# Optimization experiments

Hardware: AMD Instinct MI355X
Metric: run time of the kernel (lower is better)

## Reference

```python
import jax, jax.numpy as jnp
import numpy as np

B, T, D_IN, H, A, DEPTH = 64, 256, 256, 512, 128, 4


def hsig(v):
    # Keras hard_sigmoid
    return jnp.clip(0.2 * v + 0.5, 0.0, 1.0)


def setup_inputs() -> dict:
    key = jax.random.key(0)
    ks = jax.random.split(key, 8)
    s = 0.02
    return {
        "x": jax.random.normal(ks[0], (B, T, D_IN), jnp.float32),
        "mask": jnp.ones((B, T), jnp.float32),
        "bucket_size": T,
        "W_emb": jax.random.normal(ks[1], (D_IN, H), jnp.float32) * s,
        "b_emb": jnp.zeros((H,), jnp.float32),
        "W": jax.random.normal(ks[2], (H, 3 * H), jnp.float32) * s,
        "U": jax.random.normal(ks[3], (H, 3 * H), jnp.float32) * s,
        "b": jnp.zeros((3 * H,), jnp.float32),
        "W_action_1": jax.random.normal(ks[4], (H, A), jnp.float32) * s,
        "U_action_1": jax.random.normal(ks[5], (H, A), jnp.float32) * s,
        "b_action_1": jnp.zeros((A,), jnp.float32),
        "W_action_2": jax.random.normal(ks[6], (A, 2), jnp.float32) * s,
        "b_action_2": jnp.zeros((2,), jnp.float32),
    }


def _forward(x, mask, bucket_size, W_emb, b_emb, W, U, b,
             W_action_1, U_action_1, b_action_1, W_action_2, b_action_2):
    Bn, Tn = x.shape[0], int(bucket_size)
    Hn = W_emb.shape[1]
    f32 = x.dtype

    dm = mask.T[:Tn]                                   # [T,B]
    eos = dm * (1.0 - jnp.concatenate([dm[1:], jnp.zeros((1, Bn), f32)], 0))
    seos = jnp.concatenate([jnp.zeros((1, Bn), f32), eos[:-1]], 0)
    xe = (jnp.einsum('btd,dh->tbh', x, W_emb) + b_emb)[:Tn]  # [T,B,H]
    llm3 = jnp.concatenate([jnp.zeros((DEPTH - 1, Bn), f32), jnp.ones((1, Bn), f32)], 0)

    Wz, Wr, Wh = W[:, :Hn], W[:, Hn:2 * Hn], W[:, 2 * Hn:]
    Uz, Ur, Uh = U[:, :Hn], U[:, Hn:2 * Hn], U[:, 2 * Hn:]
    bz, br, bh = b[:Hn], b[Hn:2 * Hn], b[2 * Hn:]

    def vert_step(carry, llm):
        x_d, ap_d, dm_d = carry                        # [T,B,H],[T,B],[T,B]
        sdm = jnp.concatenate([jnp.ones((1, Bn), f32), dm_d[:-1]], 0)

        def horiz(c, s):
            h_tm1, a_tm1, dmc_tm1 = c
            xt, ap, dmp_tm1, dmp, e_tm1 = s
            pol_h = jax.nn.relu(xt @ W_action_1 + h_tm1 @ U_action_1 + b_action_1)
            pol = jnp.exp(pol_h @ W_action_2 + b_action_2)          # [B,2]
            act = (pol[:, 0] >= pol[:, 1]).astype(f32)
            act = jnp.where(ap > 0, 1.0, act)
            act = jnp.where(llm > 0, 1.0, act)
            act = jnp.where(e_tm1 > 0, 0.0, act)
            act_calc = dmp_tm1 * (1 - llm) * (1 - e_tm1) * (1 - ap)
            z = hsig(xt @ Wz + h_tm1 @ Uz + bz)
            r = hsig(xt @ Wr + h_tm1 @ Ur + br)
            h_cand = z * h_tm1 + (1 - z) * jnp.tanh(xt @ Wh + (r * h_tm1) @ Uh + bh)
            both = (1 - ap) * dmp * act * dmc_tm1
            h_only = dmc_tm1 * act * (ap + (1 - ap) * (1 - dmp))
            x_only = dmp * (1 - ap) * (1 - act + act * (1 - dmc_tm1))
            dm_new = both + x_only + h_only
            h = jnp.where(both[:, None] > 0, h_cand, 0.0)
            h = jnp.where(h_only[:, None] > 0, h_tm1, h)
            h = jnp.where(x_only[:, None] > 0, xt, h)
            act = jnp.where(dmp_tm1 > 0, act, a_tm1)
            dm_new = dmp * dm_new
            h = jnp.where(dmp[:, None] > 0, h, h_tm1)
            return (h, act, dm_new), (h, act, dm_new, act_calc, pol)

        init = (jnp.zeros((Bn, Hn), f32), jnp.zeros((Bn,), f32), jnp.zeros((Bn,), f32))
        _, (h, act, ndm, ac, pol) = jax.lax.scan(horiz, init, (x_d, ap_d, sdm, dm_d, seos))
        sa = jnp.concatenate([act[1:], jnp.zeros((1, Bn), f32)], 0)
        pih = jnp.concatenate([jnp.zeros((1, Bn, Hn), f32), h[1:]], 0)
        return (h, sa, ndm), (h, sa, ac, x_d, pih, pol)

    init = (xe, jnp.zeros((Tn, Bn), f32), dm)
    _, (hS, saS, acS, pixS, pihS, polS) = jax.lax.scan(vert_step, init, llm3)
    output = hS[-1, -1]                                # [B,H]
    action = jnp.transpose(saS, (2, 0, 1))             # [B,depth,T]
    action_calc = jnp.transpose(acS, (2, 0, 1))
    pix = jnp.transpose(pixS, (2, 0, 1, 3))            # [B,depth,T,H]
    pih = jnp.transpose(pihS, (2, 0, 1, 3))
    pol = jnp.transpose(polS, (2, 0, 1, 3))            # [B,depth,T,2]
    return (output, action, action_calc, pix, pih, pol)


def reference(x, mask, bucket_size, W_emb, b_emb, W, U, b,
              W_action_1, U_action_1, b_action_1, W_action_2, b_action_2):
    return _forward(x, mask, bucket_size, W_emb, b_emb, W, U, b,
                    W_action_1, U_action_1, b_action_1, W_action_2, b_action_2)
```

## Files before the change

kernel.cpp:

```cpp
#include <hip/hip_runtime.h>


#define Bn   64
#define Tn   256
#define DIN  256
#define Hn   512
#define An   128
#define DEP  4
#define N3   1536
#define NC   1664
#define NU   1152
#define THREADS 320

__device__ __forceinline__ float hsigf(float v) {
    return fminf(fmaxf(0.2f * v + 0.5f, 0.f), 1.f);
}
__device__ __forceinline__ float aloadf(const float* p) {
    return __hip_atomic_load(p, __ATOMIC_RELAXED, __HIP_MEMORY_SCOPE_AGENT);
}
__device__ __forceinline__ void astoref(float* p, float v) {
    __hip_atomic_store(p, v, __ATOMIC_RELAXED, __HIP_MEMORY_SCOPE_AGENT);
}

__global__ __launch_bounds__(256) void pack_w_k(const float* __restrict__ W,
                                                const float* __restrict__ Wa1,
                                                float* __restrict__ Wc) {
    int idx = blockIdx.x * 256 + threadIdx.x;
    if (idx >= Hn * NC) return;
    int k = idx / NC, c = idx % NC;
    Wc[idx] = (c < N3) ? W[(size_t)k * N3 + c] : Wa1[(size_t)k * An + (c - N3)];
}

__global__ __launch_bounds__(256) void pack_u_k(const float* __restrict__ U,
                                                const float* __restrict__ Ua1,
                                                float* __restrict__ Uc) {
    int idx = blockIdx.x * 256 + threadIdx.x;
    if (idx >= Hn * NU) return;
    int k = idx / NU, c = idx % NU;
    Uc[idx] = (c < 1024) ? U[(size_t)k * N3 + c] : Ua1[(size_t)k * An + (c - 1024)];
}

__global__ __launch_bounds__(256) void init_misc_k(const float* __restrict__ bb,
                                                   const float* __restrict__ ba1,
                                                   float* __restrict__ bc,
                                                   const float* __restrict__ mask,
                                                   float* __restrict__ seos,
                                                   float* __restrict__ dmh0,
                                                   float* __restrict__ o_pih,
                                                   unsigned int* __restrict__ flags) {
    int idx = blockIdx.x * 256 + threadIdx.x;
    if (idx < NC) bc[idx] = (idx < N3) ? bb[idx] : ba1[idx - N3];
    if (idx < 128) flags[idx] = 0u;
    if (idx < Tn * Bn) {
        int t = idx / Bn, b = idx % Bn;
        float m0 = mask[(size_t)b * Tn + t];
        dmh0[idx] = m0;
        float s = 0.f;
        if (t > 0) s = mask[(size_t)b * Tn + (t - 1)] * (1.f - m0);
        seos[idx] = s;
    }
    if (idx < Bn * DEP * Hn) {
        int b = idx / (DEP * Hn);
        int r = idx % (DEP * Hn);
        int d = r / Hn, h = r % Hn;
        o_pih[(((size_t)b * DEP + d) * Tn + 0) * Hn + h] = 0.f;
    }
}

__global__ __launch_bounds__(256) void gemm64_k(
    const float* __restrict__ Am, long aBase0, long aStep, long aStride,
    const float* __restrict__ Bm, int ldb, const float* __restrict__ bias,
    float* __restrict__ Cm, long cBase0, long cStep, long cStride, int K) {
    const int qm = blockIdx.x, qn = blockIdx.y;
    const long aBase = aBase0 + (long)qm * aStep;
    const long cBase = cBase0 + (long)qm * cStep;
    const int n0 = qn * 64;
    __shared__ float As[64][65];
    __shared__ float Bs[64][68];
    const int tid = threadIdx.x;
    const int tx = tid & 15, ty = tid >> 4;
    float acc[4][4] = {};
    for (int k0 = 0; k0 < K; k0 += 64) {
#pragma unroll
        for (int fi = 0; fi < 4; ++fi) {
            const int f = fi * 256 + tid;
            const int mm = f >> 4;
            const int k4 = (f & 15) << 2;
            const float4 v = *(const float4*)(Am + aBase + (long)mm * aStride + k0 + k4);
            As[k4 + 0][mm] = v.x; As[k4 + 1][mm] = v.y;
            As[k4 + 2][mm] = v.z; As[k4 + 3][mm] = v.w;
        }
#pragma unroll
        for (int fi = 0; fi < 4; ++fi) {
            const int f = fi * 256 + tid;
            const int k = f >> 4;
            const int n4 = (f & 15) << 2;
            *(float4*)&Bs[k][n4] = *(const float4*)(Bm + (long)(k0 + k) * ldb + n0 + n4);
        }
        __syncthreads();
#pragma unroll 16
        for (int k = 0; k < 64; ++k) {
            const float a0 = As[k][ty * 4 + 0];
            const float a1 = As[k][ty * 4 + 1];
            const float a2 = As[k][ty * 4 + 2];
            const float a3 = As[k][ty * 4 + 3];
            const float4 bv = *(const float4*)&Bs[k][tx * 4];
            acc[0][0] = fmaf(a0, bv.x, acc[0][0]); acc[0][1] = fmaf(a0, bv.y, acc[0][1]);
            acc[0][2] = fmaf(a0, bv.z, acc[0][2]); acc[0][3] = fmaf(a0, bv.w, acc[0][3]);
            acc[1][0] = fmaf(a1, bv.x, acc[1][0]); acc[1][1] = fmaf(a1, bv.y, acc[1][1]);
            acc[1][2] = fmaf(a1, bv.z, acc[1][2]); acc[1][3] = fmaf(a1, bv.w, acc[1][3]);
            acc[2][0] = fmaf(a2, bv.x, acc[2][0]); acc[2][1] = fmaf(a2, bv.y, acc[2][1]);
            acc[2][2] = fmaf(a2, bv.z, acc[2][2]); acc[2][3] = fmaf(a2, bv.w, acc[2][3]);
            acc[3][0] = fmaf(a3, bv.x, acc[3][0]); acc[3][1] = fmaf(a3, bv.y, acc[3][1]);
            acc[3][2] = fmaf(a3, bv.z, acc[3][2]); acc[3][3] = fmaf(a3, bv.w, acc[3][3]);
        }
        __syncthreads();
    }
#pragma unroll
    for (int i = 0; i < 4; ++i) {
        const int mm = ty * 4 + i;
        float* cp = Cm + cBase + (long)mm * cStride + n0 + tx * 4;
#pragma unroll
        for (int j = 0; j < 4; ++j) {
            float v = acc[i][j];
            if (bias) v += bias[n0 + tx * 4 + j];
            cp[j] = v;
        }
    }
}

__global__ __launch_bounds__(THREADS) void scan_chunk_k(
    const float* __restrict__ XWA, const float* __restrict__ Uc,
    const float* __restrict__ Umat, const float* __restrict__ W2,
    const float* __restrict__ b2,
    float* __restrict__ hbuf,
    float* __restrict__ G1buf,
    float* __restrict__ gatebuf,
    unsigned int* __restrict__ flags,
    const float* __restrict__ seos, float* __restrict__ dmh,
    float* __restrict__ acth,
    float* __restrict__ o_act, float* __restrict__ o_ac, float* __restrict__ o_pol,
    float* __restrict__ o_pix, float* __restrict__ o_pih, float* __restrict__ o_out,
    int d, int c) {
    const int b = blockIdx.x;
    const int s = blockIdx.y;
    const int tid = threadIdx.x;
    const int llm = (d == DEP - 1) ? 1 : 0;

    __shared__ float h_s[Hn];
    __shared__ float rh_s[Hn];
    __shared__ float red_s[4][288];
    __shared__ float ph_s[An];
    __shared__ float gate_s[4];

    unsigned int* arr1 = flags;
    unsigned int* arr2 = flags + 64;

    float a_prev = 0.f, dmc_prev = 0.f;
    if (s == 3 && tid == 0 && c > 0) {
        const int t0 = c * 64;
        a_prev   = acth[(t0 - 1) * Bn + b];
        dmc_prev = dmh[(size_t)(d + 1) * Tn * Bn + (t0 - 1) * Bn + b];
    }

    for (int tt = 0; tt < 64; ++tt) {
        const int t = c * 64 + tt;
        const int g = d * Tn + t;
        const int par = g & 1;
        const unsigned int tgt = 4u * (unsigned)(g + 1);
        const float* xrow = XWA + ((size_t)tt * Bn + b) * NC;

        float dmp_tm1 = 1.f, dmp = 0.f, ap = 0.f, e_tm1 = 0.f;
        if (s == 3 && tid == 0) {
            dmp = dmh[(size_t)d * Tn * Bn + t * Bn + b];
            if (t > 0) dmp_tm1 = dmh[(size_t)d * Tn * Bn + (t - 1) * Bn + b];
            if (d > 0) ap = o_act[(size_t)b * DEP * Tn + (d - 1) * Tn + t];
            e_tm1 = seos[t * Bn + b];
        }

        for (int k = tid; k < Hn; k += THREADS)
            h_s[k] = (t == 0) ? 0.f : aloadf(&hbuf[((size_t)par * Bn + b) * Hn + k]);
        __syncthreads();

        if (tid < 288) {
            const int gq = tid % 72, kq = tid / 72;
            const int j0 = s * 288 + 4 * gq;
            const float* wp = Uc + (size_t)(kq * 128) * NU + j0;
            float4 acc = {0.f, 0.f, 0.f, 0.f};
#pragma unroll 8
            for (int k = 0; k < 128; ++k) {
                const float4 w = *(const float4*)(wp + (size_t)k * NU);
                const float hk = h_s[kq * 128 + k];
                acc.x = fmaf(w.x, hk, acc.x); acc.y = fmaf(w.y, hk, acc.y);
                acc.z = fmaf(w.z, hk, acc.z); acc.w = fmaf(w.w, hk, acc.w);
            }
            *(float4*)&red_s[kq][4 * gq] = acc;
        }
        __syncthreads();
        float myG1 = 0.f;
        if (tid < 288) {
            myG1 = red_s[0][tid] + red_s[1][tid] + red_s[2][tid] + red_s[3][tid];
            astoref(&G1buf[(size_t)b * NU + s * 288 + tid], myG1);
        }
        if (s == 3 && tid >= 160 && tid < 288) {
            const int i = tid - 160;
            ph_s[i] = fmaxf(xrow[N3 + i] + myG1, 0.f);
        }
        __syncthreads();

        if (s == 3 && tid < 64) {
            float p0p = ph_s[tid] * W2[2 * tid]     + ph_s[tid + 64] * W2[2 * (tid + 64)];
            float p1p = ph_s[tid] * W2[2 * tid + 1] + ph_s[tid + 64] * W2[2 * (tid + 64) + 1];
            for (int off = 32; off; off >>= 1) {
                p0p += __shfl_down(p0p, off);
                p1p += __shfl_down(p1p, off);
            }
            if (tid == 0) {
                const float p0 = expf(b2[0] + p0p), p1 = expf(b2[1] + p1p);
                const float a_tm1   = (t == 0) ? 0.f : a_prev;
                const float dmc_tm1 = (t == 0) ? 0.f : dmc_prev;
                float act = (p0 >= p1) ? 1.f : 0.f;
                if (ap > 0.f) act = 1.f;
                if (llm) act = 1.f;
                if (e_tm1 > 0.f) act = 0.f;
                const float lf = llm ? 1.f : 0.f;
                const float acalc  = dmp_tm1 * (1.f - lf) * (1.f - e_tm1) * (1.f - ap);
                const float both   = (1.f - ap) * dmp * act * dmc_tm1;
                const float h_only = dmc_tm1 * act * (ap + (1.f - ap) * (1.f - dmp));
                const float x_only = dmp * (1.f - ap) * (1.f - act + act * (1.f - dmc_tm1));
                const float dm_new = dmp * (both + x_only + h_only);
                const float act_out = (dmp_tm1 > 0.f) ? act : a_tm1;
                astoref(&gatebuf[b * 8 + 0], both);
                astoref(&gatebuf[b * 8 + 1], h_only);
                astoref(&gatebuf[b * 8 + 2], x_only);
                astoref(&gatebuf[b * 8 + 3], dmp);
                dmh[(size_t)(d + 1) * Tn * Bn + t * Bn + b] = dm_new;
                o_ac[(size_t)b * DEP * Tn + d * Tn + t] = acalc;
                o_pol[((size_t)b * DEP * Tn + d * Tn + t) * 2 + 0] = p0;
                o_pol[((size_t)b * DEP * Tn + d * Tn + t) * 2 + 1] = p1;
                acth[t * Bn + b] = act_out;
                if (t > 0) o_act[(size_t)b * DEP * Tn + d * Tn + (t - 1)] = act_out;
                if (t == Tn - 1) o_act[(size_t)b * DEP * Tn + d * Tn + (Tn - 1)] = 0.f;
                a_prev = act_out; dmc_prev = dm_new;
            }
        }

        __syncthreads();
        if (tid == 0) {
            __hip_atomic_fetch_add(&arr1[b], 1u, __ATOMIC_RELAXED, __HIP_MEMORY_SCOPE_AGENT);
            while (__hip_atomic_load(&arr1[b], __ATOMIC_RELAXED, __HIP_MEMORY_SCOPE_AGENT) < tgt)
                __builtin_amdgcn_s_sleep(1);
        }
        __syncthreads();

        if (tid < 4) gate_s[tid] = aloadf(&gatebuf[b * 8 + tid]);
        for (int k = tid; k < Hn; k += THREADS) {
            const float rr = hsigf(xrow[512 + k] + aloadf(&G1buf[(size_t)b * NU + 512 + k]));
            rh_s[k] = rr * h_s[k];
        }
        __syncthreads();

        if (tid < 128) {
            const int gq = tid % 32, kq = tid / 32;
            const int j0 = 128 * s + 4 * gq;
            const float* wp = Umat + (size_t)(kq * 128) * N3 + 1024 + j0;
            float4 acc = {0.f, 0.f, 0.f, 0.f};
#pragma unroll 8
            for (int k = 0; k < 128; ++k) {
                const float4 w = *(const float4*)(wp + (size_t)k * N3);
                const float r_ = rh_s[kq * 128 + k];
                acc.x = fmaf(w.x, r_, acc.x); acc.y = fmaf(w.y, r_, acc.y);
                acc.z = fmaf(w.z, r_, acc.z); acc.w = fmaf(w.w, r_, acc.w);
            }
            *(float4*)&red_s[kq][4 * gq] = acc;
        }
        __syncthreads();

        if (tid < 128) {
            const int j = 128 * s + tid;
            const float dot = red_s[0][tid] + red_s[1][tid] + red_s[2][tid] + red_s[3][tid];
            const float z = hsigf(xrow[j] + aloadf(&G1buf[(size_t)b * NU + j]));
            const float hp = h_s[j];
            const float th = tanhf(xrow[1024 + j] + dot);
            const float hc = z * hp + (1.f - z) * th;
            const float xt = o_pix[(((size_t)b * DEP + d) * Tn + t) * Hn + j];
            const float both = gate_s[0], h_only = gate_s[1],
                        x_only = gate_s[2], dmpv = gate_s[3];
            float hv = (both > 0.f) ? hc : 0.f;
            if (h_only > 0.f) hv = hp;
            if (x_only > 0.f) hv = xt;
            if (!(dmpv > 0.f)) hv = hp;
            astoref(&hbuf[((size_t)(par ^ 1) * Bn + b) * Hn + j], hv);
            if (d < DEP - 1) o_pix[(((size_t)b * DEP + d + 1) * Tn + t) * Hn + j] = hv;
            if (t > 0)       o_pih[(((size_t)b * DEP + d) * Tn + t) * Hn + j] = hv;
            if (d == DEP - 1 && t == Tn - 1) o_out[(size_t)b * Hn + j] = hv;
        }

        __syncthreads();
        if (tid == 0) {
            __hip_atomic_fetch_add(&arr2[b], 1u, __ATOMIC_RELAXED, __HIP_MEMORY_SCOPE_AGENT);
            while (__hip_atomic_load(&arr2[b], __ATOMIC_RELAXED, __HIP_MEMORY_SCOPE_AGENT) < tgt)
                __builtin_amdgcn_s_sleep(1);
        }
        __syncthreads();
    }
}

extern "C" void kernel_launch(void* const* d_in, const int* in_sizes, int n_in,
                              void* d_out, int out_size, void* d_ws, size_t ws_size,
                              hipStream_t stream) {
    const float* x     = (const float*)d_in[0];
    const float* mask  = (const float*)d_in[1];
    const float* W_emb = (const float*)d_in[3];
    const float* b_emb = (const float*)d_in[4];
    const float* W     = (const float*)d_in[5];
    const float* U     = (const float*)d_in[6];
    const float* bb    = (const float*)d_in[7];
    const float* Wa1   = (const float*)d_in[8];
    const float* Ua1   = (const float*)d_in[9];
    const float* ba1   = (const float*)d_in[10];
    const float* W2    = (const float*)d_in[11];
    const float* b2    = (const float*)d_in[12];

    float* out = (float*)d_out;
    float* o_out = out;
    float* o_act = out + (size_t)Bn * Hn;
    float* o_ac  = o_act + (size_t)Bn * DEP * Tn;
    float* o_pix = o_ac + (size_t)Bn * DEP * Tn;
    float* o_pih = o_pix + (size_t)Bn * DEP * Tn * Hn;
    float* o_pol = o_pih + (size_t)Bn * DEP * Tn * Hn;

    float* ws      = (float*)d_ws;
    float* seos    = ws;
    float* dmh     = seos + Tn * Bn;
    float* acth    = dmh + (DEP + 1) * Tn * Bn;
    float* hbuf    = acth + Tn * Bn;
    float* G1buf   = hbuf + 2 * Bn * Hn;
    float* gatebuf = G1buf + (size_t)Bn * NU;
    unsigned int* flags = (unsigned int*)(gatebuf + Bn * 8);
    float* Wc      = gatebuf + Bn * 8 + 128;
    float* bc      = Wc + (size_t)Hn * NC;
    float* Uc      = bc + NC;
    float* XWA     = Uc + (size_t)Hn * NU;

    pack_w_k<<<(Hn * NC + 255) / 256, 256, 0, stream>>>(W, Wa1, Wc);
    pack_u_k<<<(Hn * NU + 255) / 256, 256, 0, stream>>>(U, Ua1, Uc);
    init_misc_k<<<(Bn * DEP * Hn + 255) / 256, 256, 0, stream>>>(
        bb, ba1, bc, mask, seos, dmh, o_pih, flags);

    gemm64_k<<<dim3(Tn, Hn / 64), 256, 0, stream>>>(
        x, 0L, (long)DIN, (long)Tn * DIN, W_emb, Hn, b_emb,
        o_pix, 0L, (long)Hn, (long)DEP * Tn * Hn, DIN);

    for (int d = 0; d < DEP; ++d) {
        for (int c = 0; c < 4; ++c) {
            gemm64_k<<<dim3(64, NC / 64), 256, 0, stream>>>(
                o_pix, (long)(d * Tn + c * 64) * Hn, (long)Hn, (long)DEP * Tn * Hn,
                Wc, NC, bc, XWA, 0L, (long)Bn * NC, (long)NC, Hn);
            scan_chunk_k<<<dim3(Bn, 4), THREADS, 0, stream>>>(
                XWA, Uc, U, W2, b2, hbuf, G1buf, gatebuf, flags,
                seos, dmh, acth, o_act, o_ac, o_pol, o_pix, o_pih, o_out, d, c);
        }
    }
}
```

Measured before the change: 19.51 ms.

## Regroup recurrent scan: 4 batches per block, 16 column slices, transposed U weights

The scan kernel now gives each block 4 batch rows and one of 16 column slices, not one batch row and one of 4 slices. U is pre-transposed so each thread computes a full-K dot product for one column and one batch, which removes the shared-memory partial-sum reduction and reuses each loaded weight row across 4 batches. The policy/gate computation is replicated in every slice rather than broadcast through a global gate buffer, and the time chunk is halved to 32 steps. This trades one inter-block barrier and more kernel launches for better weight reuse and more blocks per step, with 16 blocks now meeting at each flag barrier.

```diff
diff --git a/kernel.cpp b/kernel.cpp
--- a/kernel.cpp
+++ b/kernel.cpp
@@ -10,12 +10,21 @@
 #define N3   1536
 #define NC   1664
 #define NU   1152
+#define TB   (Tn * Bn)
+#define CH   32
+#define SL   16
 #define THREADS 320
+#define HS   520
+
+typedef unsigned long long ull;
 
 __device__ __forceinline__ float hsigf(float v) {
     return fminf(fmaxf(0.2f * v + 0.5f, 0.f), 1.f);
 }
 __device__ __forceinline__ float aloadf(const float* p) {
+    return __hip_atomic_load(p, __ATOMIC_RELAXED, __HIP_MEMORY_SCOPE_AGENT);
+}
+__device__ __forceinline__ ull aloadu(const ull* p) {
     return __hip_atomic_load(p, __ATOMIC_RELAXED, __HIP_MEMORY_SCOPE_AGENT);
 }
 __device__ __forceinline__ void astoref(float* p, float v) {
@@ -31,13 +40,20 @@
     Wc[idx] = (c < N3) ? W[(size_t)k * N3 + c] : Wa1[(size_t)k * An + (c - N3)];
 }
 
-__global__ __launch_bounds__(256) void pack_u_k(const float* __restrict__ U,
+__global__ __launch_bounds__(256) void pack_t_k(const float* __restrict__ U,
                                                 const float* __restrict__ Ua1,
-                                                float* __restrict__ Uc) {
+                                                float* __restrict__ UcT,
+                                                float* __restrict__ UhT) {
     int idx = blockIdx.x * 256 + threadIdx.x;
-    if (idx >= Hn * NU) return;
-    int k = idx / NU, c = idx % NU;
-    Uc[idx] = (c < 1024) ? U[(size_t)k * N3 + c] : Ua1[(size_t)k * An + (c - 1024)];
+    if (idx >= (NU + Hn) * Hn) return;
+    int col = idx >> 9, k = idx & 511;
+    if (col < NU) {
+        UcT[idx] = (col < 1024) ? U[(size_t)k * N3 + col]
+                                : Ua1[(size_t)k * An + (col - 1024)];
+    } else {
+        int j = col - NU;
+        UhT[(size_t)j * Hn + k] = U[(size_t)k * N3 + 1024 + j];
+    }
 }
 
 __global__ __launch_bounds__(256) void init_misc_k(const float* __restrict__ bb,
@@ -50,8 +66,8 @@
                                                    unsigned int* __restrict__ flags) {
     int idx = blockIdx.x * 256 + threadIdx.x;
     if (idx < NC) bc[idx] = (idx < N3) ? bb[idx] : ba1[idx - N3];
-    if (idx < 128) flags[idx] = 0u;
-    if (idx < Tn * Bn) {
+    if (idx < 2048) flags[idx] = 0u;
+    if (idx < TB) {
         int t = idx / Bn, b = idx % Bn;
         float m0 = mask[(size_t)b * Tn + t];
         dmh0[idx] = m0;
@@ -130,176 +146,191 @@
 }
 
 __global__ __launch_bounds__(THREADS) void scan_chunk_k(
-    const float* __restrict__ XWA, const float* __restrict__ Uc,
-    const float* __restrict__ Umat, const float* __restrict__ W2,
+    const float* __restrict__ XWA, const float* __restrict__ UcT,
+    const float* __restrict__ UhT, const float* __restrict__ W2,
     const float* __restrict__ b2,
     float* __restrict__ hbuf,
     float* __restrict__ G1buf,
-    float* __restrict__ gatebuf,
     unsigned int* __restrict__ flags,
     const float* __restrict__ seos, float* __restrict__ dmh,
     float* __restrict__ acth,
     float* __restrict__ o_act, float* __restrict__ o_ac, float* __restrict__ o_pol,
     float* __restrict__ o_pix, float* __restrict__ o_pih, float* __restrict__ o_out,
     int d, int c) {
-    const int b = blockIdx.x;
-    const int s = blockIdx.y;
+    const int s = blockIdx.x;
+    const int q = blockIdx.y;
+    const int B0 = q * 4;
     const int tid = threadIdx.x;
+    const int wv = tid >> 6, ln = tid & 63;
     const int llm = (d == DEP - 1) ? 1 : 0;
 
-    __shared__ float h_s[Hn];
-    __shared__ float rh_s[Hn];
-    __shared__ float red_s[4][288];
-    __shared__ float ph_s[An];
-    __shared__ float gate_s[4];
-
-    unsigned int* arr1 = flags;
-    unsigned int* arr2 = flags + 64;
-
-    float a_prev = 0.f, dmc_prev = 0.f;
-    if (s == 3 && tid == 0 && c > 0) {
-        const int t0 = c * 64;
-        a_prev   = acth[(t0 - 1) * Bn + b];
-        dmc_prev = dmh[(size_t)(d + 1) * Tn * Bn + (t0 - 1) * Bn + b];
-    }
-
-    for (int tt = 0; tt < 64; ++tt) {
-        const int t = c * 64 + tt;
+    __shared__ float h_s[4][HS];
+    __shared__ float rh_s[4][HS];
+    __shared__ float gate_s[4][4];
+    __shared__ float pa_s[4][2];
+    __shared__ float w2_s[2 * An];
+    __shared__ float b2_s[2];
+
+    unsigned int* f1 = flags + q * 64;
+    unsigned int* f2 = flags + 1024 + q * 64;
+
+    for (int i = tid; i < 2 * An; i += THREADS) w2_s[i] = W2[i];
+    if (tid < 2) b2_s[tid] = b2[tid];
+    if (tid < 4) {
+        float ap_ = 0.f, dp_ = 0.f;
+        if (c > 0) {
+            const int t0 = c * CH;
+            ap_ = acth[(t0 - 1) * Bn + B0 + tid];
+            dp_ = dmh[(size_t)(d + 1) * TB + (t0 - 1) * Bn + B0 + tid];
+        }
+        pa_s[tid][0] = ap_; pa_s[tid][1] = dp_;
+    }
+    __syncthreads();
+
+    for (int tt = 0; tt < CH; ++tt) {
+        const int t = c * CH + tt;
         const int g = d * Tn + t;
         const int par = g & 1;
-        const unsigned int tgt = 4u * (unsigned)(g + 1);
-        const float* xrow = XWA + ((size_t)tt * Bn + b) * NC;
-
-        float dmp_tm1 = 1.f, dmp = 0.f, ap = 0.f, e_tm1 = 0.f;
-        if (s == 3 && tid == 0) {
-            dmp = dmh[(size_t)d * Tn * Bn + t * Bn + b];
-            if (t > 0) dmp_tm1 = dmh[(size_t)d * Tn * Bn + (t - 1) * Bn + b];
-            if (d > 0) ap = o_act[(size_t)b * DEP * Tn + (d - 1) * Tn + t];
-            e_tm1 = seos[t * Bn + b];
-        }
-
-        for (int k = tid; k < Hn; k += THREADS)
-            h_s[k] = (t == 0) ? 0.f : aloadf(&hbuf[((size_t)par * Bn + b) * Hn + k]);
+        const unsigned int tgt = 16u * (unsigned)(g + 1);
+
+        float dmp = 0.f, dmp1 = 1.f, ap = 0.f, eos1 = 0.f;
+        if (wv < 4 && ln == 0) {
+            const int gb = B0 + wv;
+            dmp = dmh[(size_t)d * TB + t * Bn + gb];
+            if (t > 0) dmp1 = dmh[(size_t)d * TB + (t - 1) * Bn + gb];
+            if (d > 0) ap = o_act[(size_t)gb * DEP * Tn + (d - 1) * Tn + t];
+            eos1 = seos[t * Bn + gb];
+        }
+
+        if (t == 0) {
+            for (int idx = tid; idx < 4 * Hn; idx += THREADS)
+                h_s[idx >> 9][idx & 511] = 0.f;
+        } else {
+            for (int idx = tid; idx < 4 * (Hn / 2); idx += THREADS) {
+                const int b = idx >> 8, kk = (idx & 255) * 2;
+                const ull v = aloadu((const ull*)&hbuf[((size_t)par * Bn + B0 + b) * Hn + kk]);
+                h_s[b][kk]     = __uint_as_float((unsigned)v);
+                h_s[b][kk + 1] = __uint_as_float((unsigned)(v >> 32));
+            }
+        }
         __syncthreads();
 
         if (tid < 288) {
-            const int gq = tid % 72, kq = tid / 72;
-            const int j0 = s * 288 + 4 * gq;
-            const float* wp = Uc + (size_t)(kq * 128) * NU + j0;
-            float4 acc = {0.f, 0.f, 0.f, 0.f};
+            const int c1 = tid >> 2, b = tid & 3;
+            const int gcol = s * 72 + c1;
+            const float* wp = UcT + (size_t)gcol * Hn;
+            float4 a4 = {0.f, 0.f, 0.f, 0.f};
 #pragma unroll 8
-            for (int k = 0; k < 128; ++k) {
-                const float4 w = *(const float4*)(wp + (size_t)k * NU);
-                const float hk = h_s[kq * 128 + k];
-                acc.x = fmaf(w.x, hk, acc.x); acc.y = fmaf(w.y, hk, acc.y);
-                acc.z = fmaf(w.z, hk, acc.z); acc.w = fmaf(w.w, hk, acc.w);
-            }
-            *(float4*)&red_s[kq][4 * gq] = acc;
-        }
-        __syncthreads();
-        float myG1 = 0.f;
-        if (tid < 288) {
-            myG1 = red_s[0][tid] + red_s[1][tid] + red_s[2][tid] + red_s[3][tid];
-            astoref(&G1buf[(size_t)b * NU + s * 288 + tid], myG1);
-        }
-        if (s == 3 && tid >= 160 && tid < 288) {
-            const int i = tid - 160;
-            ph_s[i] = fmaxf(xrow[N3 + i] + myG1, 0.f);
-        }
-        __syncthreads();
-
-        if (s == 3 && tid < 64) {
-            float p0p = ph_s[tid] * W2[2 * tid]     + ph_s[tid + 64] * W2[2 * (tid + 64)];
-            float p1p = ph_s[tid] * W2[2 * tid + 1] + ph_s[tid + 64] * W2[2 * (tid + 64) + 1];
+            for (int k4 = 0; k4 < Hn; k4 += 4) {
+                const float4 w = *(const float4*)(wp + k4);
+                const float4 h = *(const float4*)&h_s[b][k4];
+                a4.x = fmaf(w.x, h.x, a4.x); a4.y = fmaf(w.y, h.y, a4.y);
+                a4.z = fmaf(w.z, h.z, a4.z); a4.w = fmaf(w.w, h.w, a4.w);
+            }
+            astoref(&G1buf[(size_t)(B0 + b) * NU + gcol],
+                    (a4.x + a4.y) + (a4.z + a4.w));
+        }
+
+        __syncthreads();
+        if (tid == 0) {
+            __hip_atomic_fetch_add(f1, 1u, __ATOMIC_RELAXED, __HIP_MEMORY_SCOPE_AGENT);
+            while (__hip_atomic_load(f1, __ATOMIC_RELAXED, __HIP_MEMORY_SCOPE_AGENT) < tgt)
+                __builtin_amdgcn_s_sleep(1);
+        }
+        __syncthreads();
+
+        if (wv < 4) {
+            const int gb = B0 + wv;
+            const float* xr = XWA + ((size_t)tt * Bn + gb) * NC;
+            const float g0 = aloadf(&G1buf[(size_t)gb * NU + 1024 + ln]);
+            const float g1 = aloadf(&G1buf[(size_t)gb * NU + 1024 + 64 + ln]);
+            const float ph0 = fmaxf(xr[N3 + ln] + g0, 0.f);
+            const float ph1 = fmaxf(xr[N3 + 64 + ln] + g1, 0.f);
+            float p0p = ph0 * w2_s[2 * ln]     + ph1 * w2_s[2 * (64 + ln)];
+            float p1p = ph0 * w2_s[2 * ln + 1] + ph1 * w2_s[2 * (64 + ln) + 1];
             for (int off = 32; off; off >>= 1) {
                 p0p += __shfl_down(p0p, off);
                 p1p += __shfl_down(p1p, off);
             }
-            if (tid == 0) {
-                const float p0 = expf(b2[0] + p0p), p1 = expf(b2[1] + p1p);
-                const float a_tm1   = (t == 0) ? 0.f : a_prev;
-                const float dmc_tm1 = (t == 0) ? 0.f : dmc_prev;
+            if (ln == 0) {
+                const float p0 = expf(b2_s[0] + p0p), p1 = expf(b2_s[1] + p1p);
+                const float a_tm1   = (t == 0) ? 0.f : pa_s[wv][0];
+                const float dmc_tm1 = (t == 0) ? 0.f : pa_s[wv][1];
                 float act = (p0 >= p1) ? 1.f : 0.f;
                 if (ap > 0.f) act = 1.f;
                 if (llm) act = 1.f;
-                if (e_tm1 > 0.f) act = 0.f;
+                if (eos1 > 0.f) act = 0.f;
                 const float lf = llm ? 1.f : 0.f;
-                const float acalc  = dmp_tm1 * (1.f - lf) * (1.f - e_tm1) * (1.f - ap);
+                const float acalc  = dmp1 * (1.f - lf) * (1.f - eos1) * (1.f - ap);
                 const float both   = (1.f - ap) * dmp * act * dmc_tm1;
                 const float h_only = dmc_tm1 * act * (ap + (1.f - ap) * (1.f - dmp));
                 const float x_only = dmp * (1.f - ap) * (1.f - act + act * (1.f - dmc_tm1));
                 const float dm_new = dmp * (both + x_only + h_only);
-                const float act_out = (dmp_tm1 > 0.f) ? act : a_tm1;
-                astoref(&gatebuf[b * 8 + 0], both);
-                astoref(&gatebuf[b * 8 + 1], h_only);
-                astoref(&gatebuf[b * 8 + 2], x_only);
-                astoref(&gatebuf[b * 8 + 3], dmp);
-                dmh[(size_t)(d + 1) * Tn * Bn + t * Bn + b] = dm_new;
-                o_ac[(size_t)b * DEP * Tn + d * Tn + t] = acalc;
-                o_pol[((size_t)b * DEP * Tn + d * Tn + t) * 2 + 0] = p0;
-                o_pol[((size_t)b * DEP * Tn + d * Tn + t) * 2 + 1] = p1;
-                acth[t * Bn + b] = act_out;
-                if (t > 0) o_act[(size_t)b * DEP * Tn + d * Tn + (t - 1)] = act_out;
-                if (t == Tn - 1) o_act[(size_t)b * DEP * Tn + d * Tn + (Tn - 1)] = 0.f;
-                a_prev = act_out; dmc_prev = dm_new;
-            }
-        }
-
-        __syncthreads();
-        if (tid == 0) {
-            __hip_atomic_fetch_add(&arr1[b], 1u, __ATOMIC_RELAXED, __HIP_MEMORY_SCOPE_AGENT);
-            while (__hip_atomic_load(&arr1[b], __ATOMIC_RELAXED, __HIP_MEMORY_SCOPE_AGENT) < tgt)
-                __builtin_amdgcn_s_sleep(1);
-        }
-        __syncthreads();
-
-        if (tid < 4) gate_s[tid] = aloadf(&gatebuf[b * 8 + tid]);
-        for (int k = tid; k < Hn; k += THREADS) {
-            const float rr = hsigf(xrow[512 + k] + aloadf(&G1buf[(size_t)b * NU + 512 + k]));
-            rh_s[k] = rr * h_s[k];
+                const float act_out = (dmp1 > 0.f) ? act : a_tm1;
+                gate_s[wv][0] = both; gate_s[wv][1] = h_only;
+                gate_s[wv][2] = x_only; gate_s[wv][3] = dmp;
+                pa_s[wv][0] = act_out; pa_s[wv][1] = dm_new;
+                if (s == 0) {
+                    acth[t * Bn + gb] = act_out;
+                    dmh[(size_t)(d + 1) * TB + t * Bn + gb] = dm_new;
+                    o_ac[(size_t)gb * DEP * Tn + d * Tn + t] = acalc;
+                    o_pol[((size_t)gb * DEP * Tn + d * Tn + t) * 2 + 0] = p0;
+                    o_pol[((size_t)gb * DEP * Tn + d * Tn + t) * 2 + 1] = p1;
+                    if (t > 0) o_act[(size_t)gb * DEP * Tn + d * Tn + (t - 1)] = act_out;
+                    if (t == Tn - 1) o_act[(size_t)gb * DEP * Tn + d * Tn + (Tn - 1)] = 0.f;
+                }
+            }
+        }
+
+        for (int idx = tid; idx < 4 * (Hn / 2); idx += THREADS) {
+            const int b = idx >> 8, kk = (idx & 255) * 2;
+            const int gb = B0 + b;
+            const ull gv = aloadu((const ull*)&G1buf[(size_t)gb * NU + 512 + kk]);
+            const float* xr = XWA + ((size_t)tt * Bn + gb) * NC + 512 + kk;
+            const float r0 = hsigf(xr[0] + __uint_as_float((unsigned)gv));
+            const float r1 = hsigf(xr[1] + __uint_as_float((unsigned)(gv >> 32)));
+            rh_s[b][kk]     = r0 * h_s[b][kk];
+            rh_s[b][kk + 1] = r1 * h_s[b][kk + 1];
         }
         __syncthreads();
 
         if (tid < 128) {
-            const int gq = tid % 32, kq = tid / 32;
-            const int j0 = 128 * s + 4 * gq;
-            const float* wp = Umat + (size_t)(kq * 128) * N3 + 1024 + j0;
-            float4 acc = {0.f, 0.f, 0.f, 0.f};
+            const int c2 = tid >> 2, b = tid & 3;
+            const int gj = s * 32 + c2;
+            const int gb = B0 + b;
+            const float* xr = XWA + ((size_t)tt * Bn + gb) * NC;
+            const float zg = aloadf(&G1buf[(size_t)gb * NU + gj]);
+            const float xt = o_pix[(((size_t)gb * DEP + d) * Tn + t) * Hn + gj];
+            const float* wp = UhT + (size_t)gj * Hn;
+            float4 a4 = {0.f, 0.f, 0.f, 0.f};
 #pragma unroll 8
-            for (int k = 0; k < 128; ++k) {
-                const float4 w = *(const float4*)(wp + (size_t)k * N3);
-                const float r_ = rh_s[kq * 128 + k];
-                acc.x = fmaf(w.x, r_, acc.x); acc.y = fmaf(w.y, r_, acc.y);
-                acc.z = fmaf(w.z, r_, acc.z); acc.w = fmaf(w.w, r_, acc.w);
-            }
-            *(float4*)&red_s[kq][4 * gq] = acc;
-        }
-        __syncthreads();
-
-        if (tid < 128) {
-            const int j = 128 * s + tid;
-            const float dot = red_s[0][tid] + red_s[1][tid] + red_s[2][tid] + red_s[3][tid];
-            const float z = hsigf(xrow[j] + aloadf(&G1buf[(size_t)b * NU + j]));
-            const float hp = h_s[j];
-            const float th = tanhf(xrow[1024 + j] + dot);
+            for (int k4 = 0; k4 < Hn; k4 += 4) {
+                const float4 w = *(const float4*)(wp + k4);
+                const float4 r = *(const float4*)&rh_s[b][k4];
+                a4.x = fmaf(w.x, r.x, a4.x); a4.y = fmaf(w.y, r.y, a4.y);
+                a4.z = fmaf(w.z, r.z, a4.z); a4.w = fmaf(w.w, r.w, a4.w);
+            }
+            const float dot = (a4.x + a4.y) + (a4.z + a4.w);
+            const float z = hsigf(xr[gj] + zg);
+            const float hp = h_s[b][gj];
+            const float th = tanhf(xr[1024 + gj] + dot);
             const float hc = z * hp + (1.f - z) * th;
-            const float xt = o_pix[(((size_t)b * DEP + d) * Tn + t) * Hn + j];
-            const float both = gate_s[0], h_only = gate_s[1],
-                        x_only = gate_s[2], dmpv = gate_s[3];
+            const float both = gate_s[b][0], h_only = gate_s[b][1],
+                        x_only = gate_s[b][2], dmpv = gate_s[b][3];
             float hv = (both > 0.f) ? hc : 0.f;
             if (h_only > 0.f) hv = hp;
             if (x_only > 0.f) hv = xt;
             if (!(dmpv > 0.f)) hv = hp;
-            astoref(&hbuf[((size_t)(par ^ 1) * Bn + b) * Hn + j], hv);
-            if (d < DEP - 1) o_pix[(((size_t)b * DEP + d + 1) * Tn + t) * Hn + j] = hv;
-            if (t > 0)       o_pih[(((size_t)b * DEP + d) * Tn + t) * Hn + j] = hv;
-            if (d == DEP - 1 && t == Tn - 1) o_out[(size_t)b * Hn + j] = hv;
+            astoref(&hbuf[((size_t)(par ^ 1) * Bn + gb) * Hn + gj], hv);
+            if (d < DEP - 1) o_pix[(((size_t)gb * DEP + d + 1) * Tn + t) * Hn + gj] = hv;
+            if (t > 0)       o_pih[(((size_t)gb * DEP + d) * Tn + t) * Hn + gj] = hv;
+            if (d == DEP - 1 && t == Tn - 1) o_out[(size_t)gb * Hn + gj] = hv;
         }
 
         __syncthreads();
         if (tid == 0) {
-            __hip_atomic_fetch_add(&arr2[b], 1u, __ATOMIC_RELAXED, __HIP_MEMORY_SCOPE_AGENT);
-            while (__hip_atomic_load(&arr2[b], __ATOMIC_RELAXED, __HIP_MEMORY_SCOPE_AGENT) < tgt)
+            __hip_atomic_fetch_add(f2, 1u, __ATOMIC_RELAXED, __HIP_MEMORY_SCOPE_AGENT);
+            while (__hip_atomic_load(f2, __ATOMIC_RELAXED, __HIP_MEMORY_SCOPE_AGENT) < tgt)
                 __builtin_amdgcn_s_sleep(1);
         }
         __syncthreads();
@@ -332,19 +363,19 @@
 
     float* ws      = (float*)d_ws;
     float* seos    = ws;
-    float* dmh     = seos + Tn * Bn;
-    float* acth    = dmh + (DEP + 1) * Tn * Bn;
-    float* hbuf    = acth + Tn * Bn;
+    float* dmh     = seos + TB;
+    float* acth    = dmh + (DEP + 1) * TB;
+    float* hbuf    = acth + TB;
     float* G1buf   = hbuf + 2 * Bn * Hn;
-    float* gatebuf = G1buf + (size_t)Bn * NU;
-    unsigned int* flags = (unsigned int*)(gatebuf + Bn * 8);
-    float* Wc      = gatebuf + Bn * 8 + 128;
+    unsigned int* flags = (unsigned int*)(G1buf + (size_t)Bn * NU);
+    float* Wc      = (float*)(flags + 2048);
     float* bc      = Wc + (size_t)Hn * NC;
-    float* Uc      = bc + NC;
-    float* XWA     = Uc + (size_t)Hn * NU;
+    float* UcT     = bc + NC;
+    float* UhT     = UcT + (size_t)NU * Hn;
+    float* XWA     = UhT + (size_t)Hn * Hn;
 
     pack_w_k<<<(Hn * NC + 255) / 256, 256, 0, stream>>>(W, Wa1, Wc);
-    pack_u_k<<<(Hn * NU + 255) / 256, 256, 0, stream>>>(U, Ua1, Uc);
+    pack_t_k<<<((NU + Hn) * Hn + 255) / 256, 256, 0, stream>>>(U, Ua1, UcT, UhT);
     init_misc_k<<<(Bn * DEP * Hn + 255) / 256, 256, 0, stream>>>(
         bb, ba1, bc, mask, seos, dmh, o_pih, flags);
 
@@ -353,12 +384,12 @@
         o_pix, 0L, (long)Hn, (long)DEP * Tn * Hn, DIN);
 
     for (int d = 0; d < DEP; ++d) {
-        for (int c = 0; c < 4; ++c) {
-            gemm64_k<<<dim3(64, NC / 64), 256, 0, stream>>>(
-                o_pix, (long)(d * Tn + c * 64) * Hn, (long)Hn, (long)DEP * Tn * Hn,
+        for (int c = 0; c < Tn / CH; ++c) {
+            gemm64_k<<<dim3(CH, NC / 64), 256, 0, stream>>>(
+                o_pix, (long)(d * Tn + c * CH) * Hn, (long)Hn, (long)DEP * Tn * Hn,
                 Wc, NC, bc, XWA, 0L, (long)Bn * NC, (long)NC, Hn);
-            scan_chunk_k<<<dim3(Bn, 4), THREADS, 0, stream>>>(
-                XWA, Uc, U, W2, b2, hbuf, G1buf, gatebuf, flags,
+            scan_chunk_k<<<dim3(SL, 16), THREADS, 0, stream>>>(
+                XWA, UcT, UhT, W2, b2, hbuf, G1buf, flags,
                 seos, dmh, acth, o_act, o_ac, o_pol, o_pix, o_pih, o_out, d, c);
         }
     }
```

Measured after the change: 22.49 ms. +15.3%, slower.
